# Optimization experiments

Measured on AMD Instinct MI355X. Metric: run time of the kernel, lower is better.

The kernel has to match this reference:

```python
import jax, jax.numpy as jnp
import numpy as np

NUM_BLOCKS = 2
RES_LAYERS = 10
HID = 128
IN_CH = 256
MID_CH = 512
OUT_CH = 256
DILATIONS = [2 ** l for b in range(NUM_BLOCKS) for l in range(RES_LAYERS)]
GOOD = sum(DILATIONS)  # 2046
NLAYERS = NUM_BLOCKS * RES_LAYERS


def setup_inputs() -> dict:
    key = jax.random.key(0)
    ks = jax.random.split(key, 16)
    s = 0.05
    B, T = 8, 8192
    inp = {
        "inputs": jax.random.normal(ks[0], (B, IN_CH, T), dtype=jnp.float32),
        "Wi": jax.random.normal(ks[1], (HID, IN_CH), dtype=jnp.float32) * s,
        "bi": jax.random.normal(ks[2], (HID,), dtype=jnp.float32) * s,
        "Wf": jax.random.normal(ks[3], (NLAYERS, HID, HID, 2), dtype=jnp.float32) * s,
        "bf": jax.random.normal(ks[4], (NLAYERS, HID), dtype=jnp.float32) * s,
        "Wg": jax.random.normal(ks[5], (NLAYERS, HID, HID, 2), dtype=jnp.float32) * s,
        "bg": jax.random.normal(ks[6], (NLAYERS, HID), dtype=jnp.float32) * s,
        "Wr": jax.random.normal(ks[7], (NLAYERS, HID, HID), dtype=jnp.float32) * s,
        "br": jax.random.normal(ks[8], (NLAYERS, HID), dtype=jnp.float32) * s,
        "W1": jax.random.normal(ks[9], (MID_CH, HID), dtype=jnp.float32) * s,
        "b1": jax.random.normal(ks[10], (MID_CH,), dtype=jnp.float32) * s,
        "W2": jax.random.normal(ks[11], (OUT_CH, MID_CH), dtype=jnp.float32) * s,
        "b2": jax.random.normal(ks[12], (OUT_CH,), dtype=jnp.float32) * s,
    }
    return inp


def _dilated_k2(x, W, b, d):
    # x: [B, C, T] -> [B, C, T-d]
    y = jnp.einsum("oi,bit->bot", W[:, :, 0], x[:, :, :-d]) \
        + jnp.einsum("oi,bit->bot", W[:, :, 1], x[:, :, d:])
    return y + b[None, :, None]


def reference(inputs, Wi, bi, Wf, bf, Wg, bg, Wr, br, W1, b1, W2, b2):
    T = inputs.shape[2]
    target = T - GOOD
    res = jnp.einsum("oi,bit->bot", Wi, inputs) + bi[None, :, None]
    final = None
    for idx, d in enumerate(DILATIONS):
        f = jnp.tanh(_dilated_k2(res, Wf[idx], bf[idx], d))
        g = jax.nn.sigmoid(_dilated_k2(res, Wg[idx], bg[idx], d))
        out = f * g
        x = jnp.einsum("oi,bit->bot", Wr[idx], out) + br[idx][None, :, None]
        res = x + res[:, :, d:]
        # NOTE: original code computes split conv then immediately overwrites
        # it with x[:, :, -target:]; the split conv is dead code, so skip it.
        skip = x[:, :, -target:]
        final = skip if final is None else final + skip
    h = jax.nn.relu(final)
    h = jnp.einsum("oi,bit->bot", W1, h) + b1[None, :, None]
    h = jax.nn.relu(h)
    h = jnp.einsum("oi,bit->bot", W2, h) + b2[None, :, None]
    n, c, l = h.shape
    return jnp.transpose(h, (0, 2, 1)).reshape(n * l, c)
```

## Files before the change

### kernel.cpp

```cpp
#include <hip/hip_runtime.h>


#define TT 8192
#define HIDC 128
#define GOODC 2046
#define TGT 6146
#define NL 20
#define TILE 128
#define NTB 64
#define NTILES 512
#define NBLK 512
#define GATE_CAP (1 << 18)
#define RDV_CAP (1 << 16)

typedef _Float16 half8_t __attribute__((ext_vector_type(8)));
typedef _Float16 half4_t __attribute__((ext_vector_type(4)));
typedef float floatx4 __attribute__((ext_vector_type(4)));

__device__ int g_progress[NTILES];
__device__ int g_qhead[8];
__device__ int g_arrive;
__device__ int g_broken;

__device__ __forceinline__ floatx4 mfma16(half8_t a, half8_t b, floatx4 c) {
  return __builtin_amdgcn_mfma_f32_16x16x32_f16(a, b, c, 0, 0, 0);
}
__device__ __forceinline__ float fast_sigmoid(float x) {
  return __builtin_amdgcn_rcpf(1.0f + __expf(-x));
}
__device__ __forceinline__ float fast_tanh(float x) {
  return 2.0f * __builtin_amdgcn_rcpf(1.0f + __expf(-2.0f * x)) - 1.0f;
}

__device__ __forceinline__ void cload8(
    const void* p0, const void* p1, const void* p2, const void* p3,
    const void* p4, const void* p5, const void* p6, const void* p7,
    floatx4& r0, floatx4& r1, floatx4& r2, floatx4& r3,
    floatx4& r4, floatx4& r5, floatx4& r6, floatx4& r7) {
  asm volatile(
      "global_load_dwordx4 %0, %8, off sc0\n\t"
      "global_load_dwordx4 %1, %9, off sc0\n\t"
      "global_load_dwordx4 %2, %10, off sc0\n\t"
      "global_load_dwordx4 %3, %11, off sc0\n\t"
      "global_load_dwordx4 %4, %12, off sc0\n\t"
      "global_load_dwordx4 %5, %13, off sc0\n\t"
      "global_load_dwordx4 %6, %14, off sc0\n\t"
      "global_load_dwordx4 %7, %15, off sc0\n\t"
      "s_waitcnt vmcnt(0)"
      : "=&v"(r0), "=&v"(r1), "=&v"(r2), "=&v"(r3),
        "=&v"(r4), "=&v"(r5), "=&v"(r6), "=&v"(r7)
      : "v"(p0), "v"(p1), "v"(p2), "v"(p3),
        "v"(p4), "v"(p5), "v"(p6), "v"(p7)
      : "memory");
}
__device__ __forceinline__ void cload4(const void* p0, const void* p1,
                                       const void* p2, const void* p3,
                                       floatx4& r0, floatx4& r1, floatx4& r2,
                                       floatx4& r3) {
  asm volatile(
      "global_load_dwordx4 %0, %4, off sc0\n\t"
      "global_load_dwordx4 %1, %5, off sc0\n\t"
      "global_load_dwordx4 %2, %6, off sc0\n\t"
      "global_load_dwordx4 %3, %7, off sc0\n\t"
      "s_waitcnt vmcnt(0)"
      : "=&v"(r0), "=&v"(r1), "=&v"(r2), "=&v"(r3)
      : "v"(p0), "v"(p1), "v"(p2), "v"(p3)
      : "memory");
}

__device__ __forceinline__ void spin_tile(int idx, int q) {
  int* f = &g_progress[idx];
  int it = 0;
  while (__hip_atomic_load(f, __ATOMIC_RELAXED, __HIP_MEMORY_SCOPE_AGENT) < q) {
    if (!(++it & 15) && __hip_atomic_load(&g_broken, __ATOMIC_RELAXED,
                                          __HIP_MEMORY_SCOPE_AGENT))
      break;
    if (it > GATE_CAP) {
      __hip_atomic_store(&g_broken, 1, __ATOMIC_RELAXED,
                         __HIP_MEMORY_SCOPE_AGENT);
      break;
    }
    __builtin_amdgcn_s_sleep(1);
  }
}

__global__ void prep_kernel(const float* __restrict__ Wi, const float* __restrict__ Wf,
                            const float* __restrict__ Wg, const float* __restrict__ Wr,
                            const float* __restrict__ W1, const float* __restrict__ W2,
                            _Float16* __restrict__ WIh, _Float16* __restrict__ WFG,
                            _Float16* __restrict__ WRh, _Float16* __restrict__ W1h,
                            _Float16* __restrict__ W2h) {
  int idx = blockIdx.x * blockDim.x + threadIdx.x;
  int stride = gridDim.x * blockDim.x;
  for (int i = idx; i < NTILES; i += stride) g_progress[i] = 0;
  for (int i = idx; i < 8; i += stride) g_qhead[i] = 0;
  if (idx == 0) { g_arrive = 0; g_broken = 0; }
  for (int i = idx; i < NL * 256 * 256; i += stride) {
    int l = i >> 16; int m = (i >> 8) & 255; int k = i & 255;
    int tap = k >> 7; int ci = k & 127;
    float v;
    if (m < 128) v = Wf[(((size_t)l * 128 + m) * 128 + ci) * 2 + tap];
    else         v = Wg[(((size_t)l * 128 + (m - 128)) * 128 + ci) * 2 + tap];
    WFG[i] = (_Float16)v;
  }
  for (int i = idx; i < NL * 128 * 128; i += stride) WRh[i] = (_Float16)Wr[i];
  for (int i = idx; i < 128 * 256; i += stride) WIh[i] = (_Float16)Wi[i];
  for (int i = idx; i < 512 * 128; i += stride) W1h[i] = (_Float16)W1[i];
  for (int i = idx; i < 256 * 512; i += stride) W2h[i] = (_Float16)W2[i];
}

__device__ __forceinline__ void input_half(
    const float* __restrict__ ib, const _Float16* __restrict__ WIh,
    const float* __restrict__ bi, _Float16* __restrict__ R0g,
    _Float16* __restrict__ pbout, int u0t, int h, char* smem) {
  _Float16(*Rown)[136] = (_Float16(*)[136])smem;
  _Float16(*Xs)[264] = (_Float16(*)[264])(smem + 34816);
  const int u0 = u0t + 64 * h;
  const int tid = threadIdx.x;
  const int lane = tid & 63;
  const int w = tid >> 6;
  const int ml = lane & 15;
  const int mq = lane >> 4;

#pragma unroll
  for (int it = 0; it < 4; ++it) {
    int i = it * 256 + tid;
    int n4 = i & 15;
    int kg = i >> 4;
    const float* src = ib + (size_t)(kg * 4) * TT + u0 + n4 * 4;
    floatx4 c0 = *(const floatx4*)(src);
    floatx4 c1 = *(const floatx4*)(src + TT);
    floatx4 c2 = *(const floatx4*)(src + 2 * TT);
    floatx4 c3 = *(const floatx4*)(src + 3 * TT);
#pragma unroll
    for (int tq = 0; tq < 4; ++tq) {
      half4_t hh;
      hh[0] = (_Float16)c0[tq]; hh[1] = (_Float16)c1[tq];
      hh[2] = (_Float16)c2[tq]; hh[3] = (_Float16)c3[tq];
      *(half4_t*)&Xs[n4 * 4 + tq][kg * 4] = hh;
    }
  }
  __syncthreads();

  floatx4 acc[2][4];
#pragma unroll
  for (int a = 0; a < 2; ++a)
#pragma unroll
    for (int c = 0; c < 4; ++c) acc[a][c] = floatx4{0.f, 0.f, 0.f, 0.f};
  const _Float16* Aw = WIh + (size_t)(32 * w + ml) * 256;
#pragma unroll
  for (int kk = 0; kk < 8; ++kk) {
    const int ko = kk * 32 + mq * 8;
    half8_t a0 = *(const half8_t*)(Aw + ko);
    half8_t a1 = *(const half8_t*)(Aw + 16 * 256 + ko);
#pragma unroll
    for (int nt = 0; nt < 4; ++nt) {
      half8_t bv = *(const half8_t*)&Xs[nt * 16 + ml][ko];
      acc[0][nt] = mfma16(a0, bv, acc[0][nt]);
      acc[1][nt] = mfma16(a1, bv, acc[1][nt]);
    }
  }
  __syncthreads();
  float* Xf = (float*)(smem + 34816);
#pragma unroll
  for (int mt = 0; mt < 2; ++mt) {
    const int mb = 32 * w + mt * 16 + mq * 4;
#pragma unroll
    for (int nt = 0; nt < 4; ++nt)
      *(floatx4*)&Xf[(nt * 16 + ml) * 132 + mb] = acc[mt][nt];
  }
  __syncthreads();
#pragma unroll
  for (int it = 0; it < 4; ++it) {
    int i = it * 256 + tid;
    int n = i >> 4; int cq = i & 15;
    floatx4 x0 = *(const floatx4*)&Xf[n * 132 + cq * 8];
    floatx4 x1 = *(const floatx4*)&Xf[n * 132 + cq * 8 + 4];
    floatx4 b0 = *(const floatx4*)(bi + cq * 8);
    floatx4 b1v = *(const floatx4*)(bi + cq * 8 + 4);
    half8_t hh;
#pragma unroll
    for (int tq = 0; tq < 4; ++tq) {
      hh[tq] = (_Float16)(x0[tq] + b0[tq]);
      hh[4 + tq] = (_Float16)(x1[tq] + b1v[tq]);
    }
    *(half8_t*)&Rown[64 * h + n][cq * 8] = hh;
    *(half8_t*)(R0g + (size_t)(u0 + n) * HIDC + cq * 8) = hh;
    if (h == 1 && n == 63)
      *(half8_t*)(pbout + (size_t)(u0 + n) * HIDC + cq * 8) = hh;
  }
  __syncthreads();
}

__device__ __forceinline__ void phase_layer(
    const _Float16* __restrict__ pbin, _Float16* __restrict__ pbout,
    const _Float16* __restrict__ WFGl, const _Float16* __restrict__ WRl,
    const float* __restrict__ bfl, const float* __restrict__ bgl,
    const float* __restrict__ brl, int d, int u0, int ext, char* smem) {
  _Float16(*Rown)[136] = (_Float16(*)[136])smem;
  _Float16(*Xs0)[136] = (_Float16(*)[136])(smem + 34816);
  const int tid = threadIdx.x;
  const int lane = tid & 63;
  const int w = tid >> 6;
  const int ml = lane & 15;
  const int mq = lane >> 4;

  const int dd = d < TILE ? d : TILE;
  const int nch = dd << 4;
  {
    const void* sp[8];
#pragma unroll
    for (int k = 0; k < 8; ++k) {
      int i = tid + (k << 8);
      int row = i >> 4, cc = i & 15;
      int p = u0 - d + row;
      if (p < 0) p = 0;
      sp[k] = (i < nch) ? (const void*)(pbin + (size_t)p * HIDC + cc * 8)
                        : (const void*)pbin;
    }
    floatx4 rr0, rr1, rr2, rr3, rr4, rr5, rr6, rr7;
    cload8(sp[0], sp[1], sp[2], sp[3], sp[4], sp[5], sp[6], sp[7],
           rr0, rr1, rr2, rr3, rr4, rr5, rr6, rr7);
    floatx4 rr[8] = {rr0, rr1, rr2, rr3, rr4, rr5, rr6, rr7};
#pragma unroll
    for (int k = 0; k < 8; ++k) {
      int i = tid + (k << 8);
      if (i < nch) *(floatx4*)&Xs0[i >> 4][(i & 15) * 8] = rr[k];
    }
  }
  __syncthreads();

  const _Float16* brow0[8];
  const _Float16* brow1[8];
#pragma unroll
  for (int nt = 0; nt < 8; ++nt) {
    int n = nt * 16 + ml;
    brow1[nt] = &Rown[n][0];
    brow0[nt] = (n < dd) ? &Xs0[n][0] : &Rown[n - d][0];
  }

  floatx4 accF[2][8], accG[2][8];
#pragma unroll
  for (int a = 0; a < 2; ++a)
#pragma unroll
    for (int cc = 0; cc < 8; ++cc) {
      accF[a][cc] = floatx4{0.f, 0.f, 0.f, 0.f};
      accG[a][cc] = floatx4{0.f, 0.f, 0.f, 0.f};
    }
  const _Float16* Af = WFGl + (size_t)(32 * w + ml) * 256;
  const _Float16* Ag = Af + 128 * 256;
#pragma unroll
  for (int h = 0; h < 2; ++h) {
#pragma unroll
    for (int kk = 0; kk < 4; ++kk) {
      const int ko = kk * 32 + mq * 8;
      const int kw = h * 128 + ko;
      half8_t aF0 = *(const half8_t*)(Af + kw);
      half8_t aF1 = *(const half8_t*)(Af + 16 * 256 + kw);
      half8_t aG0 = *(const half8_t*)(Ag + kw);
      half8_t aG1 = *(const half8_t*)(Ag + 16 * 256 + kw);
#pragma unroll
      for (int nt = 0; nt < 8; ++nt) {
        half8_t bv = *(const half8_t*)((h ? brow1[nt] : brow0[nt]) + ko);
        accF[0][nt] = mfma16(aF0, bv, accF[0][nt]);
        accF[1][nt] = mfma16(aF1, bv, accF[1][nt]);
        accG[0][nt] = mfma16(aG0, bv, accG[0][nt]);
        accG[1][nt] = mfma16(aG1, bv, accG[1][nt]);
      }
    }
  }

  half4_t og[2][8];
#pragma unroll
  for (int mt = 0; mt < 2; ++mt) {
    const int mb = 32 * w + mt * 16 + mq * 4;
    floatx4 bfv = *(const floatx4*)(bfl + mb);
    floatx4 bgv = *(const floatx4*)(bgl + mb);
#pragma unroll
    for (int nt = 0; nt < 8; ++nt) {
#pragma unroll
      for (int r = 0; r < 4; ++r) {
        float fv = fast_tanh(accF[mt][nt][r] + bfv[r]);
        float gv = fast_sigmoid(accG[mt][nt][r] + bgv[r]);
        og[mt][nt][r] = (_Float16)(fv * gv);
      }
    }
  }
  __syncthreads();

  _Float16(*Os)[136] = Xs0;
#pragma unroll
  for (int mt = 0; mt < 2; ++mt) {
    const int mb = 32 * w + mt * 16 + mq * 4;
#pragma unroll
    for (int nt = 0; nt < 8; ++nt)
      *(half4_t*)&Os[nt * 16 + ml][mb] = og[mt][nt];
  }
  __syncthreads();

  floatx4 accX[2][8];
#pragma unroll
  for (int a = 0; a < 2; ++a)
#pragma unroll
    for (int cc = 0; cc < 8; ++cc) accX[a][cc] = floatx4{0.f, 0.f, 0.f, 0.f};
  const _Float16* Ar = WRl + (size_t)(32 * w + ml) * 128;
#pragma unroll
  for (int kk = 0; kk < 4; ++kk) {
    const int ko = kk * 32 + mq * 8;
    half8_t a0 = *(const half8_t*)(Ar + ko);
    half8_t a1 = *(const half8_t*)(Ar + 16 * 128 + ko);
#pragma unroll
    for (int nt = 0; nt < 8; ++nt) {
      half8_t bv = *(const half8_t*)&Os[nt * 16 + ml][ko];
      accX[0][nt] = mfma16(a0, bv, accX[0][nt]);
      accX[1][nt] = mfma16(a1, bv, accX[1][nt]);
    }
  }

  half4_t xo[2][8];
#pragma unroll
  for (int mt = 0; mt < 2; ++mt) {
    const int mb = 32 * w + mt * 16 + mq * 4;
    floatx4 brv = *(const floatx4*)(brl + mb);
#pragma unroll
    for (int nt = 0; nt < 8; ++nt) {
      const int n = nt * 16 + ml;
      half4_t rold = *(const half4_t*)&Rown[n][mb];
#pragma unroll
      for (int r = 0; r < 4; ++r)
        xo[mt][nt][r] = (_Float16)(accX[mt][nt][r] + brv[r] + (float)rold[r]);
    }
  }
  __syncthreads();

#pragma unroll
  for (int mt = 0; mt < 2; ++mt) {
    const int mb = 32 * w + mt * 16 + mq * 4;
#pragma unroll
    for (int nt = 0; nt < 8; ++nt)
      *(half4_t*)&Rown[nt * 16 + ml][mb] = xo[mt][nt];
  }
  __syncthreads();

  for (int i = tid; i < (ext << 4); i += 256) {
    int row = TILE - ext + (i >> 4);
    int cc = i & 15;
    *(half8_t*)(pbout + (size_t)(u0 + row) * HIDC + cc * 8) =
        *(const half8_t*)&Rown[row][cc * 8];
  }
}

__device__ __forceinline__ void head_half(
    const _Float16* __restrict__ R0g, const _Float16* __restrict__ W1h,
    const _Float16* __restrict__ W2h, const float* __restrict__ b1,
    const float* __restrict__ b2, float* __restrict__ outb, int u0t, int h,
    char* smem) {
  _Float16(*Rown)[136] = (_Float16(*)[136])smem;
  _Float16* Hs = (_Float16*)(smem + 34816);
  _Float16* H1s = (_Float16*)(smem + 34816 + 17408);
  const int u0 = u0t + 64 * h;
  const int tid = threadIdx.x;
  const int lane = tid & 63;
  const int w = tid >> 6;
  const int ml = lane & 15;
  const int mq = lane >> 4;

  {
    const void* sp[4];
#pragma unroll
    for (int it = 0; it < 4; ++it) {
      int i = it * 256 + tid;
      sp[it] = R0g + (size_t)(u0 + (i >> 4)) * HIDC + (i & 15) * 8;
    }
    floatx4 z0, z1, z2, z3;
    cload4(sp[0], sp[1], sp[2], sp[3], z0, z1, z2, z3);
    floatx4 zz[4] = {z0, z1, z2, z3};
#pragma unroll
    for (int it = 0; it < 4; ++it) {
      int i = it * 256 + tid;
      int n = i >> 4; int cq = i & 15;
      half8_t a = *(const half8_t*)&Rown[64 * h + n][cq * 8];
      half8_t zv = *(half8_t*)&zz[it];
      half8_t hh;
#pragma unroll
      for (int tq = 0; tq < 8; ++tq) {
        float v = (float)a[tq] - (float)zv[tq];
        hh[tq] = (_Float16)(v > 0.f ? v : 0.f);
      }
      *(half8_t*)&Hs[n * 136 + cq * 8] = hh;
    }
  }
  __syncthreads();

  floatx4 accO[4][4];
#pragma unroll
  for (int a = 0; a < 4; ++a)
#pragma unroll
    for (int c = 0; c < 4; ++c) accO[a][c] = floatx4{0.f, 0.f, 0.f, 0.f};

  for (int p = 0; p < 4; ++p) {
    floatx4 acc1[2][4];
#pragma unroll
    for (int a = 0; a < 2; ++a)
#pragma unroll
      for (int c = 0; c < 4; ++c) acc1[a][c] = floatx4{0.f, 0.f, 0.f, 0.f};
    const _Float16* A1 = W1h + (size_t)(128 * p + 32 * w + ml) * 128;
#pragma unroll
    for (int kk = 0; kk < 4; ++kk) {
      const int ko = kk * 32 + mq * 8;
      half8_t av0 = *(const half8_t*)(A1 + ko);
      half8_t av1 = *(const half8_t*)(A1 + 16 * 128 + ko);
#pragma unroll
      for (int nt = 0; nt < 4; ++nt) {
        half8_t bv = *(const half8_t*)&Hs[(nt * 16 + ml) * 136 + ko];
        acc1[0][nt] = mfma16(av0, bv, acc1[0][nt]);
        acc1[1][nt] = mfma16(av1, bv, acc1[1][nt]);
      }
    }
    __syncthreads();
#pragma unroll
    for (int mt = 0; mt < 2; ++mt) {
      const int kc = 32 * w + mt * 16 + mq * 4;
      floatx4 bv = *(const floatx4*)(b1 + 128 * p + kc);
#pragma unroll
      for (int nt = 0; nt < 4; ++nt) {
        half4_t hh;
#pragma unroll
        for (int r = 0; r < 4; ++r) {
          float v = acc1[mt][nt][r] + bv[r];
          hh[r] = (_Float16)(v > 0.f ? v : 0.f);
        }
        *(half4_t*)&H1s[(nt * 16 + ml) * 136 + kc] = hh;
      }
    }
    __syncthreads();
    const _Float16* A2 = W2h + (size_t)(64 * w + ml) * 512 + p * 128;
#pragma unroll
    for (int kk = 0; kk < 4; ++kk) {
      const int ko = kk * 32 + mq * 8;
#pragma unroll
      for (int nt = 0; nt < 4; ++nt) {
        half8_t bv = *(const half8_t*)&H1s[(nt * 16 + ml) * 136 + ko];
#pragma unroll
        for (int mt = 0; mt < 4; ++mt) {
          half8_t av = *(const half8_t*)(A2 + (size_t)(mt * 16) * 512 + ko);
          accO[mt][nt] = mfma16(av, bv, accO[mt][nt]);
        }
      }
    }
    __syncthreads();
  }

  _Float16* Ot = (_Float16*)(smem + 34816);
#pragma unroll
  for (int mt = 0; mt < 4; ++mt) {
    const int m = 64 * w + mt * 16 + mq * 4;
    floatx4 bv = *(const floatx4*)(b2 + m);
#pragma unroll
    for (int nt = 0; nt < 4; ++nt) {
      const int n = nt * 16 + ml;
      half4_t hh;
#pragma unroll
      for (int r = 0; r < 4; ++r) hh[r] = (_Float16)(accO[mt][nt][r] + bv[r]);
      *(half4_t*)&Ot[n * 264 + m] = hh;
    }
  }
  __syncthreads();
#pragma unroll
  for (int it = 0; it < 8; ++it) {
    int i = it * 256 + tid;
    int n = i >> 5;
    int g = i & 31;
    int u = u0 + n;
    if (u >= GOODC) {
      half8_t v = *(const half8_t*)&Ot[n * 264 + g * 8];
      float* dst = outb + (size_t)(u - GOODC) * 256 + g * 8;
      floatx4 v0, v1;
#pragma unroll
      for (int tq = 0; tq < 4; ++tq) { v0[tq] = (float)v[tq]; v1[tq] = (float)v[4 + tq]; }
      *(floatx4*)dst = v0;
      *(floatx4*)(dst + 4) = v1;
    }
  }
  __syncthreads();
}

__global__ __launch_bounds__(256, 2) void mega_kernel(
    const float* __restrict__ inp, const _Float16* __restrict__ WIh,
    const float* __restrict__ bi, const _Float16* __restrict__ WFG,
    const _Float16* __restrict__ WRh, const float* __restrict__ bf,
    const float* __restrict__ bg, const float* __restrict__ br,
    const _Float16* __restrict__ W1h, const _Float16* __restrict__ W2h,
    const float* __restrict__ b1, const float* __restrict__ b2,
    _Float16* __restrict__ R0g, _Float16* __restrict__ Ph,
    _Float16* __restrict__ Qh, float* __restrict__ out) {
  __shared__ __align__(16) char smem[69632];
  __shared__ int s_j, s_bb, s_light;
  const int tid = threadIdx.x;

  if (tid == 0) {
    unsigned xcd;
    asm volatile("s_getreg_b32 %0, hwreg(HW_REG_XCC_ID)" : "=s"(xcd));
    xcd &= 7;
    int slot = __hip_atomic_fetch_add(&g_qhead[xcd], 1, __ATOMIC_RELAXED,
                                      __HIP_MEMORY_SCOPE_AGENT);
    __hip_atomic_fetch_add(&g_arrive, 1, __ATOMIC_RELEASE,
                           __HIP_MEMORY_SCOPE_AGENT);
    int ok = 1, it = 0;
    while (__hip_atomic_load(&g_arrive, __ATOMIC_ACQUIRE,
                             __HIP_MEMORY_SCOPE_AGENT) < NBLK) {
      if (++it > RDV_CAP) {
        ok = 0;
        __hip_atomic_store(&g_broken, 1, __ATOMIC_RELAXED,
                           __HIP_MEMORY_SCOPE_AGENT);
        break;
      }
      __builtin_amdgcn_s_sleep(8);
    }
    int light = ok;
    if (ok) {
#pragma unroll
      for (int x = 0; x < 8; ++x)
        light &= (__hip_atomic_load(&g_qhead[x], __ATOMIC_RELAXED,
                                    __HIP_MEMORY_SCOPE_AGENT) == NBLK / 8);
    }
    if (light) { s_bb = (int)xcd; s_j = slot; }
    else       { s_bb = blockIdx.x >> 6; s_j = blockIdx.x & 63; }
    s_light = light;
  }
  __syncthreads();
  const int j = s_j;
  const int bb = s_bb;
  const int light = s_light;
  const int u0 = j * TILE;

  _Float16* R0b = R0g + (size_t)bb * TT * HIDC;
  _Float16* Phb = Ph + (size_t)bb * TT * HIDC;
  _Float16* Qhb = Qh + (size_t)bb * TT * HIDC;
  const float* ib = inp + (size_t)bb * 256 * TT;
  float* outb = out + (size_t)bb * TGT * 256;
  int* myflag = &g_progress[bb * NTB + j];

#pragma unroll 1
  for (int q = 0; q < 22; ++q) {
    if (q >= 1 && q <= 20) {
      const int dcur = 1 << ((q - 1) % 10);
      const int jraw = j - ((dcur + TILE - 1) >> 7);
      int jwar = -1;
      if (q >= 2) {
        const int dp = 1 << ((q - 2) % 10);
        int cand = j + ((dp + TILE - 1) >> 7);
        if (cand <= NTB - 1) jwar = cand;
      }
      if (tid == 0 && jraw >= 0) spin_tile(bb * NTB + jraw, q);
      if (tid == 1 && jwar >= 0) spin_tile(bb * NTB + jwar, q);
      __syncthreads();
      if (!light) __builtin_amdgcn_fence(__ATOMIC_ACQUIRE, "agent");
    }

    if (q == 0) {
      input_half(ib, WIh, bi, R0b, Qhb, u0, 0, smem);
      input_half(ib, WIh, bi, R0b, Qhb, u0, 1, smem);
    } else if (q <= 20) {
      const int l = q - 1;
      const int d = 1 << (l % 10);
      const _Float16* pbin = ((q - 1) & 1) ? Phb : Qhb;
      _Float16* pbout = (q & 1) ? Phb : Qhb;
      int ext = 0;
      if (q <= 19) {
        ext = 1 << (q % 10);
        if (ext > TILE) ext = TILE;
      }
      phase_layer(pbin, pbout, WFG + (size_t)l * 65536,
                  WRh + (size_t)l * 16384, bf + l * 128, bg + l * 128,
                  br + l * 128, d, u0, ext, smem);
    } else {
      if (u0 + 127 >= GOODC) {
        if (u0 + 63 >= GOODC)
          head_half(R0b, W1h, W2h, b1, b2, outb, u0, 0, smem);
        head_half(R0b, W1h, W2h, b1, b2, outb, u0, 1, smem);
      }
    }

    if (q <= 20) {
      if (light) {
        asm volatile("s_waitcnt vmcnt(0)" ::: "memory");
      } else {
        __builtin_amdgcn_fence(__ATOMIC_RELEASE, "agent");
      }
      __syncthreads();
      if (tid == 0)
        __hip_atomic_store(myflag, q + 1, __ATOMIC_RELAXED,
                           __HIP_MEMORY_SCOPE_AGENT);
    }
  }
}

extern "C" void kernel_launch(void* const* d_in, const int* in_sizes, int n_in,
                              void* d_out, int out_size, void* d_ws, size_t ws_size,
                              hipStream_t stream) {
  const float* inputs = (const float*)d_in[0];
  const float* Wi = (const float*)d_in[1];
  const float* bi = (const float*)d_in[2];
  const float* Wf = (const float*)d_in[3];
  const float* bf = (const float*)d_in[4];
  const float* Wg = (const float*)d_in[5];
  const float* bg = (const float*)d_in[6];
  const float* Wr = (const float*)d_in[7];
  const float* br = (const float*)d_in[8];
  const float* W1 = (const float*)d_in[9];
  const float* b1 = (const float*)d_in[10];
  const float* W2 = (const float*)d_in[11];
  const float* b2 = (const float*)d_in[12];
  float* out = (float*)d_out;

  char* ws = (char*)d_ws;
  _Float16* R0g = (_Float16*)(ws + 0);
  _Float16* Ph  = (_Float16*)(ws + 16777216);
  _Float16* Qh  = (_Float16*)(ws + 33554432);
  _Float16* WFG = (_Float16*)(ws + 50331648);
  _Float16* WRh = (_Float16*)(ws + 52953088);
  _Float16* WIh = (_Float16*)(ws + 53608448);
  _Float16* W1h = (_Float16*)(ws + 53673984);
  _Float16* W2h = (_Float16*)(ws + 53805056);

  prep_kernel<<<dim3(512), dim3(256), 0, stream>>>(Wi, Wf, Wg, Wr, W1, W2,
                                                   WIh, WFG, WRh, W1h, W2h);
  mega_kernel<<<dim3(NBLK), dim3(256), 0, stream>>>(
      inputs, WIh, bi, WFG, WRh, bf, bg, br, W1h, W2h, b1, b2,
      R0g, Ph, Qh, out);
}
```

Baseline: 834.7 us.

## Triple-buffer halo slabs to relax WAR dependencies and store halos directly from registers

Adds a third ping-pong slab for the per-layer halo exchange when the workspace is large enough. A tile then waits on its downstream neighbour's progress from one layer further back, which loosens the write-after-read gate. The halo rows are written to global memory straight from registers instead of through an extra shared-memory pass and sync. It also uses the input-projection buffer directly as the layer-1 input, checks the broken flag less often while spinning, and skips the last flag store. This adds workspace-size-dependent behaviour and a more complex dependency calculation that must stay correct.

```diff
diff --git a/kernel.cpp b/kernel.cpp
--- a/kernel.cpp
+++ b/kernel.cpp
@@ -72,8 +72,8 @@
   int* f = &g_progress[idx];
   int it = 0;
   while (__hip_atomic_load(f, __ATOMIC_RELAXED, __HIP_MEMORY_SCOPE_AGENT) < q) {
-    if (!(++it & 15) && __hip_atomic_load(&g_broken, __ATOMIC_RELAXED,
-                                          __HIP_MEMORY_SCOPE_AGENT))
+    if (!(++it & 255) && __hip_atomic_load(&g_broken, __ATOMIC_RELAXED,
+                                           __HIP_MEMORY_SCOPE_AGENT))
       break;
     if (it > GATE_CAP) {
       __hip_atomic_store(&g_broken, 1, __ATOMIC_RELAXED,
@@ -112,7 +112,7 @@
 __device__ __forceinline__ void input_half(
     const float* __restrict__ ib, const _Float16* __restrict__ WIh,
     const float* __restrict__ bi, _Float16* __restrict__ R0g,
-    _Float16* __restrict__ pbout, int u0t, int h, char* smem) {
+    int u0t, int h, char* smem) {
   _Float16(*Rown)[136] = (_Float16(*)[136])smem;
   _Float16(*Xs)[264] = (_Float16(*)[264])(smem + 34816);
   const int u0 = u0t + 64 * h;
@@ -186,8 +186,6 @@
     }
     *(half8_t*)&Rown[64 * h + n][cq * 8] = hh;
     *(half8_t*)(R0g + (size_t)(u0 + n) * HIDC + cq * 8) = hh;
-    if (h == 1 && n == 63)
-      *(half8_t*)(pbout + (size_t)(u0 + n) * HIDC + cq * 8) = hh;
   }
   __syncthreads();
 }
@@ -331,6 +329,18 @@
         xo[mt][nt][r] = (_Float16)(accX[mt][nt][r] + brv[r] + (float)rold[r]);
     }
   }
+  if (ext > 0) {
+#pragma unroll
+    for (int mt = 0; mt < 2; ++mt) {
+      const int mb = 32 * w + mt * 16 + mq * 4;
+#pragma unroll
+      for (int nt = 0; nt < 8; ++nt) {
+        const int n = nt * 16 + ml;
+        if (n >= TILE - ext)
+          *(half4_t*)(pbout + (size_t)(u0 + n) * HIDC + mb) = xo[mt][nt];
+      }
+    }
+  }
   __syncthreads();
 
 #pragma unroll
@@ -339,14 +349,6 @@
 #pragma unroll
     for (int nt = 0; nt < 8; ++nt)
       *(half4_t*)&Rown[nt * 16 + ml][mb] = xo[mt][nt];
-  }
-  __syncthreads();
-
-  for (int i = tid; i < (ext << 4); i += 256) {
-    int row = TILE - ext + (i >> 4);
-    int cc = i & 15;
-    *(half8_t*)(pbout + (size_t)(u0 + row) * HIDC + cc * 8) =
-        *(const half8_t*)&Rown[row][cc * 8];
   }
 }
 
@@ -492,8 +494,9 @@
     const float* __restrict__ bg, const float* __restrict__ br,
     const _Float16* __restrict__ W1h, const _Float16* __restrict__ W2h,
     const float* __restrict__ b1, const float* __restrict__ b2,
-    _Float16* __restrict__ R0g, _Float16* __restrict__ Ph,
-    _Float16* __restrict__ Qh, float* __restrict__ out) {
+    _Float16* __restrict__ R0g, _Float16* __restrict__ Ah,
+    _Float16* __restrict__ Bh, _Float16* __restrict__ Ch,
+    float* __restrict__ out, int nslots) {
   __shared__ __align__(16) char smem[69632];
   __shared__ int s_j, s_bb, s_light;
   const int tid = threadIdx.x;
@@ -535,8 +538,8 @@
   const int u0 = j * TILE;
 
   _Float16* R0b = R0g + (size_t)bb * TT * HIDC;
-  _Float16* Phb = Ph + (size_t)bb * TT * HIDC;
-  _Float16* Qhb = Qh + (size_t)bb * TT * HIDC;
+  _Float16* sl[3] = {Ah + (size_t)bb * TT * HIDC, Bh + (size_t)bb * TT * HIDC,
+                     Ch + (size_t)bb * TT * HIDC};
   const float* ib = inp + (size_t)bb * 256 * TT;
   float* outb = out + (size_t)bb * TGT * 256;
   int* myflag = &g_progress[bb * NTB + j];
@@ -544,28 +547,29 @@
 #pragma unroll 1
   for (int q = 0; q < 22; ++q) {
     if (q >= 1 && q <= 20) {
-      const int dcur = 1 << ((q - 1) % 10);
-      const int jraw = j - ((dcur + TILE - 1) >> 7);
-      int jwar = -1;
-      if (q >= 2) {
-        const int dp = 1 << ((q - 2) % 10);
+      const int dq = 1 << ((q - 1) % 10);
+      const int jraw = j - ((dq + TILE - 1) >> 7);
+      int jwar = -1, warq = 0;
+      if (q > nslots) {
+        const int p = q - nslots + 1;
+        const int dp = 1 << ((p - 1) % 10);
         int cand = j + ((dp + TILE - 1) >> 7);
-        if (cand <= NTB - 1) jwar = cand;
+        if (cand <= NTB - 1) { jwar = cand; warq = q - nslots + 2; }
       }
       if (tid == 0 && jraw >= 0) spin_tile(bb * NTB + jraw, q);
-      if (tid == 1 && jwar >= 0) spin_tile(bb * NTB + jwar, q);
+      if (tid == 1 && jwar >= 0) spin_tile(bb * NTB + jwar, warq);
       __syncthreads();
       if (!light) __builtin_amdgcn_fence(__ATOMIC_ACQUIRE, "agent");
     }
 
     if (q == 0) {
-      input_half(ib, WIh, bi, R0b, Qhb, u0, 0, smem);
-      input_half(ib, WIh, bi, R0b, Qhb, u0, 1, smem);
+      input_half(ib, WIh, bi, R0b, u0, 0, smem);
+      input_half(ib, WIh, bi, R0b, u0, 1, smem);
     } else if (q <= 20) {
       const int l = q - 1;
       const int d = 1 << (l % 10);
-      const _Float16* pbin = ((q - 1) & 1) ? Phb : Qhb;
-      _Float16* pbout = (q & 1) ? Phb : Qhb;
+      const _Float16* pbin = (q == 1) ? R0b : sl[(q - 2) % nslots];
+      _Float16* pbout = sl[(q - 1) % nslots];
       int ext = 0;
       if (q <= 19) {
         ext = 1 << (q % 10);
@@ -589,7 +593,7 @@
         __builtin_amdgcn_fence(__ATOMIC_RELEASE, "agent");
       }
       __syncthreads();
-      if (tid == 0)
+      if (q <= 19 && tid == 0)
         __hip_atomic_store(myflag, q + 1, __ATOMIC_RELAXED,
                            __HIP_MEMORY_SCOPE_AGENT);
     }
@@ -614,19 +618,23 @@
   const float* b2 = (const float*)d_in[12];
   float* out = (float*)d_out;
 
+  const size_t SLAB = 16777216;
+  int nslots = (ws_size >= 4 * SLAB + 4194304) ? 3 : 2;
   char* ws = (char*)d_ws;
   _Float16* R0g = (_Float16*)(ws + 0);
-  _Float16* Ph  = (_Float16*)(ws + 16777216);
-  _Float16* Qh  = (_Float16*)(ws + 33554432);
-  _Float16* WFG = (_Float16*)(ws + 50331648);
-  _Float16* WRh = (_Float16*)(ws + 52953088);
-  _Float16* WIh = (_Float16*)(ws + 53608448);
-  _Float16* W1h = (_Float16*)(ws + 53673984);
-  _Float16* W2h = (_Float16*)(ws + 53805056);
+  _Float16* Ah  = (_Float16*)(ws + SLAB);
+  _Float16* Bh  = (_Float16*)(ws + 2 * SLAB);
+  _Float16* Ch  = (_Float16*)(ws + (nslots == 3 ? 3 * SLAB : 2 * SLAB));
+  char* wb = ws + (size_t)(nslots == 3 ? 4 : 3) * SLAB;
+  _Float16* WFG = (_Float16*)(wb);
+  _Float16* WRh = (_Float16*)(wb + 2621440);
+  _Float16* WIh = (_Float16*)(wb + 3276800);
+  _Float16* W1h = (_Float16*)(wb + 3342336);
+  _Float16* W2h = (_Float16*)(wb + 3473408);
 
   prep_kernel<<<dim3(512), dim3(256), 0, stream>>>(Wi, Wf, Wg, Wr, W1, W2,
                                                    WIh, WFG, WRh, W1h, W2h);
   mega_kernel<<<dim3(NBLK), dim3(256), 0, stream>>>(
       inputs, WIh, bi, WFG, WRh, bf, bg, br, W1h, W2h, b1, b2,
-      R0g, Ph, Qh, out);
-}
+      R0g, Ah, Bh, Ch, out, nslots);
+}
```

Measured after the change: 895.4 us. 1.07x slower.

## Halve time tile to 64 and run 1024 persistent blocks with padded flags

Applied to the files above, without the earlier changes.

Shrinks each block's time tile from 128 to 64 columns and doubles the grid to 1024 blocks at 4 blocks per CU, cutting shared memory per block in half. The layer halo is now written straight from registers, the input stage no longer seeds the ping-pong buffer, and layer 1 reads R0 directly. Progress flags are padded to separate cache lines, and the broken-flag check in the spin loop runs less often. The aim is more parallelism and less false sharing on flags, at the cost of more dependency waits and more halo loads per unit of work.

```diff
diff --git a/kernel.cpp b/kernel.cpp
--- a/kernel.cpp
+++ b/kernel.cpp
@@ -6,10 +6,11 @@
 #define GOODC 2046
 #define TGT 6146
 #define NL 20
-#define TILE 128
-#define NTB 64
-#define NTILES 512
-#define NBLK 512
+#define TILE 64
+#define NTB 128
+#define NTILES 1024
+#define NBLK 1024
+#define FPAD 32
 #define GATE_CAP (1 << 18)
 #define RDV_CAP (1 << 16)
 
@@ -17,7 +18,7 @@
 typedef _Float16 half4_t __attribute__((ext_vector_type(4)));
 typedef float floatx4 __attribute__((ext_vector_type(4)));
 
-__device__ int g_progress[NTILES];
+__device__ int g_progress[NTILES * FPAD];
 __device__ int g_qhead[8];
 __device__ int g_arrive;
 __device__ int g_broken;
@@ -32,27 +33,6 @@
   return 2.0f * __builtin_amdgcn_rcpf(1.0f + __expf(-2.0f * x)) - 1.0f;
 }
 
-__device__ __forceinline__ void cload8(
-    const void* p0, const void* p1, const void* p2, const void* p3,
-    const void* p4, const void* p5, const void* p6, const void* p7,
-    floatx4& r0, floatx4& r1, floatx4& r2, floatx4& r3,
-    floatx4& r4, floatx4& r5, floatx4& r6, floatx4& r7) {
-  asm volatile(
-      "global_load_dwordx4 %0, %8, off sc0\n\t"
-      "global_load_dwordx4 %1, %9, off sc0\n\t"
-      "global_load_dwordx4 %2, %10, off sc0\n\t"
-      "global_load_dwordx4 %3, %11, off sc0\n\t"
-      "global_load_dwordx4 %4, %12, off sc0\n\t"
-      "global_load_dwordx4 %5, %13, off sc0\n\t"
-      "global_load_dwordx4 %6, %14, off sc0\n\t"
-      "global_load_dwordx4 %7, %15, off sc0\n\t"
-      "s_waitcnt vmcnt(0)"
-      : "=&v"(r0), "=&v"(r1), "=&v"(r2), "=&v"(r3),
-        "=&v"(r4), "=&v"(r5), "=&v"(r6), "=&v"(r7)
-      : "v"(p0), "v"(p1), "v"(p2), "v"(p3),
-        "v"(p4), "v"(p5), "v"(p6), "v"(p7)
-      : "memory");
-}
 __device__ __forceinline__ void cload4(const void* p0, const void* p1,
                                        const void* p2, const void* p3,
                                        floatx4& r0, floatx4& r1, floatx4& r2,
@@ -69,11 +49,11 @@
 }
 
 __device__ __forceinline__ void spin_tile(int idx, int q) {
-  int* f = &g_progress[idx];
+  int* f = &g_progress[idx * FPAD];
   int it = 0;
   while (__hip_atomic_load(f, __ATOMIC_RELAXED, __HIP_MEMORY_SCOPE_AGENT) < q) {
-    if (!(++it & 15) && __hip_atomic_load(&g_broken, __ATOMIC_RELAXED,
-                                          __HIP_MEMORY_SCOPE_AGENT))
+    if (!(++it & 255) && __hip_atomic_load(&g_broken, __ATOMIC_RELAXED,
+                                           __HIP_MEMORY_SCOPE_AGENT))
       break;
     if (it > GATE_CAP) {
       __hip_atomic_store(&g_broken, 1, __ATOMIC_RELAXED,
@@ -92,7 +72,7 @@
                             _Float16* __restrict__ W2h) {
   int idx = blockIdx.x * blockDim.x + threadIdx.x;
   int stride = gridDim.x * blockDim.x;
-  for (int i = idx; i < NTILES; i += stride) g_progress[i] = 0;
+  for (int i = idx; i < NTILES * FPAD; i += stride) g_progress[i] = 0;
   for (int i = idx; i < 8; i += stride) g_qhead[i] = 0;
   if (idx == 0) { g_arrive = 0; g_broken = 0; }
   for (int i = idx; i < NL * 256 * 256; i += stride) {
@@ -109,13 +89,13 @@
   for (int i = idx; i < 256 * 512; i += stride) W2h[i] = (_Float16)W2[i];
 }
 
-__device__ __forceinline__ void input_half(
+__device__ __forceinline__ void input_chunk(
     const float* __restrict__ ib, const _Float16* __restrict__ WIh,
     const float* __restrict__ bi, _Float16* __restrict__ R0g,
-    _Float16* __restrict__ pbout, int u0t, int h, char* smem) {
+    int u0t, int ch, char* smem) {
   _Float16(*Rown)[136] = (_Float16(*)[136])smem;
-  _Float16(*Xs)[264] = (_Float16(*)[264])(smem + 34816);
-  const int u0 = u0t + 64 * h;
+  _Float16(*Xs)[264] = (_Float16(*)[264])(smem + 17408);
+  const int u0 = u0t + 32 * ch;
   const int tid = threadIdx.x;
   const int lane = tid & 63;
   const int w = tid >> 6;
@@ -123,10 +103,10 @@
   const int mq = lane >> 4;
 
 #pragma unroll
-  for (int it = 0; it < 4; ++it) {
+  for (int it = 0; it < 2; ++it) {
     int i = it * 256 + tid;
-    int n4 = i & 15;
-    int kg = i >> 4;
+    int n4 = i & 7;
+    int kg = i >> 3;
     const float* src = ib + (size_t)(kg * 4) * TT + u0 + n4 * 4;
     floatx4 c0 = *(const floatx4*)(src);
     floatx4 c1 = *(const floatx4*)(src + TT);
@@ -142,11 +122,11 @@
   }
   __syncthreads();
 
-  floatx4 acc[2][4];
+  floatx4 acc[2][2];
 #pragma unroll
   for (int a = 0; a < 2; ++a)
 #pragma unroll
-    for (int c = 0; c < 4; ++c) acc[a][c] = floatx4{0.f, 0.f, 0.f, 0.f};
+    for (int c = 0; c < 2; ++c) acc[a][c] = floatx4{0.f, 0.f, 0.f, 0.f};
   const _Float16* Aw = WIh + (size_t)(32 * w + ml) * 256;
 #pragma unroll
   for (int kk = 0; kk < 8; ++kk) {
@@ -154,24 +134,24 @@
     half8_t a0 = *(const half8_t*)(Aw + ko);
     half8_t a1 = *(const half8_t*)(Aw + 16 * 256 + ko);
 #pragma unroll
-    for (int nt = 0; nt < 4; ++nt) {
+    for (int nt = 0; nt < 2; ++nt) {
       half8_t bv = *(const half8_t*)&Xs[nt * 16 + ml][ko];
       acc[0][nt] = mfma16(a0, bv, acc[0][nt]);
       acc[1][nt] = mfma16(a1, bv, acc[1][nt]);
     }
   }
   __syncthreads();
-  float* Xf = (float*)(smem + 34816);
+  float* Xf = (float*)(smem + 17408);
 #pragma unroll
   for (int mt = 0; mt < 2; ++mt) {
     const int mb = 32 * w + mt * 16 + mq * 4;
 #pragma unroll
-    for (int nt = 0; nt < 4; ++nt)
+    for (int nt = 0; nt < 2; ++nt)
       *(floatx4*)&Xf[(nt * 16 + ml) * 132 + mb] = acc[mt][nt];
   }
   __syncthreads();
 #pragma unroll
-  for (int it = 0; it < 4; ++it) {
+  for (int it = 0; it < 2; ++it) {
     int i = it * 256 + tid;
     int n = i >> 4; int cq = i & 15;
     floatx4 x0 = *(const floatx4*)&Xf[n * 132 + cq * 8];
@@ -184,10 +164,8 @@
       hh[tq] = (_Float16)(x0[tq] + b0[tq]);
       hh[4 + tq] = (_Float16)(x1[tq] + b1v[tq]);
     }
-    *(half8_t*)&Rown[64 * h + n][cq * 8] = hh;
+    *(half8_t*)&Rown[32 * ch + n][cq * 8] = hh;
     *(half8_t*)(R0g + (size_t)(u0 + n) * HIDC + cq * 8) = hh;
-    if (h == 1 && n == 63)
-      *(half8_t*)(pbout + (size_t)(u0 + n) * HIDC + cq * 8) = hh;
   }
   __syncthreads();
 }
@@ -198,7 +176,7 @@
     const float* __restrict__ bfl, const float* __restrict__ bgl,
     const float* __restrict__ brl, int d, int u0, int ext, char* smem) {
   _Float16(*Rown)[136] = (_Float16(*)[136])smem;
-  _Float16(*Xs0)[136] = (_Float16(*)[136])(smem + 34816);
+  _Float16(*Xs0)[136] = (_Float16(*)[136])(smem + 17408);
   const int tid = threadIdx.x;
   const int lane = tid & 63;
   const int w = tid >> 6;
@@ -208,9 +186,9 @@
   const int dd = d < TILE ? d : TILE;
   const int nch = dd << 4;
   {
-    const void* sp[8];
-#pragma unroll
-    for (int k = 0; k < 8; ++k) {
+    const void* sp[4];
+#pragma unroll
+    for (int k = 0; k < 4; ++k) {
       int i = tid + (k << 8);
       int row = i >> 4, cc = i & 15;
       int p = u0 - d + row;
@@ -218,32 +196,31 @@
       sp[k] = (i < nch) ? (const void*)(pbin + (size_t)p * HIDC + cc * 8)
                         : (const void*)pbin;
     }
-    floatx4 rr0, rr1, rr2, rr3, rr4, rr5, rr6, rr7;
-    cload8(sp[0], sp[1], sp[2], sp[3], sp[4], sp[5], sp[6], sp[7],
-           rr0, rr1, rr2, rr3, rr4, rr5, rr6, rr7);
-    floatx4 rr[8] = {rr0, rr1, rr2, rr3, rr4, rr5, rr6, rr7};
-#pragma unroll
-    for (int k = 0; k < 8; ++k) {
+    floatx4 r0, r1, r2, r3;
+    cload4(sp[0], sp[1], sp[2], sp[3], r0, r1, r2, r3);
+    floatx4 rr[4] = {r0, r1, r2, r3};
+#pragma unroll
+    for (int k = 0; k < 4; ++k) {
       int i = tid + (k << 8);
       if (i < nch) *(floatx4*)&Xs0[i >> 4][(i & 15) * 8] = rr[k];
     }
   }
   __syncthreads();
 
-  const _Float16* brow0[8];
-  const _Float16* brow1[8];
-#pragma unroll
-  for (int nt = 0; nt < 8; ++nt) {
+  const _Float16* brow0[4];
+  const _Float16* brow1[4];
+#pragma unroll
+  for (int nt = 0; nt < 4; ++nt) {
     int n = nt * 16 + ml;
     brow1[nt] = &Rown[n][0];
     brow0[nt] = (n < dd) ? &Xs0[n][0] : &Rown[n - d][0];
   }
 
-  floatx4 accF[2][8], accG[2][8];
+  floatx4 accF[2][4], accG[2][4];
 #pragma unroll
   for (int a = 0; a < 2; ++a)
 #pragma unroll
-    for (int cc = 0; cc < 8; ++cc) {
+    for (int cc = 0; cc < 4; ++cc) {
       accF[a][cc] = floatx4{0.f, 0.f, 0.f, 0.f};
       accG[a][cc] = floatx4{0.f, 0.f, 0.f, 0.f};
     }
@@ -260,7 +237,7 @@
       half8_t aG0 = *(const half8_t*)(Ag + kw);
       half8_t aG1 = *(const half8_t*)(Ag + 16 * 256 + kw);
 #pragma unroll
-      for (int nt = 0; nt < 8; ++nt) {
+      for (int nt = 0; nt < 4; ++nt) {
         half8_t bv = *(const half8_t*)((h ? brow1[nt] : brow0[nt]) + ko);
         accF[0][nt] = mfma16(aF0, bv, accF[0][nt]);
         accF[1][nt] = mfma16(aF1, bv, accF[1][nt]);
@@ -270,14 +247,14 @@
     }
   }
 
-  half4_t og[2][8];
+  half4_t og[2][4];
 #pragma unroll
   for (int mt = 0; mt < 2; ++mt) {
     const int mb = 32 * w + mt * 16 + mq * 4;
     floatx4 bfv = *(const floatx4*)(bfl + mb);
     floatx4 bgv = *(const floatx4*)(bgl + mb);
 #pragma unroll
-    for (int nt = 0; nt < 8; ++nt) {
+    for (int nt = 0; nt < 4; ++nt) {
 #pragma unroll
       for (int r = 0; r < 4; ++r) {
         float fv = fast_tanh(accF[mt][nt][r] + bfv[r]);
@@ -293,16 +270,16 @@
   for (int mt = 0; mt < 2; ++mt) {
     const int mb = 32 * w + mt * 16 + mq * 4;
 #pragma unroll
-    for (int nt = 0; nt < 8; ++nt)
+    for (int nt = 0; nt < 4; ++nt)
       *(half4_t*)&Os[nt * 16 + ml][mb] = og[mt][nt];
   }
   __syncthreads();
 
-  floatx4 accX[2][8];
+  floatx4 accX[2][4];
 #pragma unroll
   for (int a = 0; a < 2; ++a)
 #pragma unroll
-    for (int cc = 0; cc < 8; ++cc) accX[a][cc] = floatx4{0.f, 0.f, 0.f, 0.f};
+    for (int cc = 0; cc < 4; ++cc) accX[a][cc] = floatx4{0.f, 0.f, 0.f, 0.f};
   const _Float16* Ar = WRl + (size_t)(32 * w + ml) * 128;
 #pragma unroll
   for (int kk = 0; kk < 4; ++kk) {
@@ -310,20 +287,20 @@
     half8_t a0 = *(const half8_t*)(Ar + ko);
     half8_t a1 = *(const half8_t*)(Ar + 16 * 128 + ko);
 #pragma unroll
-    for (int nt = 0; nt < 8; ++nt) {
+    for (int nt = 0; nt < 4; ++nt) {
       half8_t bv = *(const half8_t*)&Os[nt * 16 + ml][ko];
       accX[0][nt] = mfma16(a0, bv, accX[0][nt]);
       accX[1][nt] = mfma16(a1, bv, accX[1][nt]);
     }
   }
 
-  half4_t xo[2][8];
+  half4_t xo[2][4];
 #pragma unroll
   for (int mt = 0; mt < 2; ++mt) {
     const int mb = 32 * w + mt * 16 + mq * 4;
     floatx4 brv = *(const floatx4*)(brl + mb);
 #pragma unroll
-    for (int nt = 0; nt < 8; ++nt) {
+    for (int nt = 0; nt < 4; ++nt) {
       const int n = nt * 16 + ml;
       half4_t rold = *(const half4_t*)&Rown[n][mb];
 #pragma unroll
@@ -331,34 +308,36 @@
         xo[mt][nt][r] = (_Float16)(accX[mt][nt][r] + brv[r] + (float)rold[r]);
     }
   }
+  if (ext > 0) {
+#pragma unroll
+    for (int mt = 0; mt < 2; ++mt) {
+      const int mb = 32 * w + mt * 16 + mq * 4;
+#pragma unroll
+      for (int nt = 0; nt < 4; ++nt) {
+        const int n = nt * 16 + ml;
+        if (n >= TILE - ext)
+          *(half4_t*)(pbout + (size_t)(u0 + n) * HIDC + mb) = xo[mt][nt];
+      }
+    }
+  }
   __syncthreads();
 
 #pragma unroll
   for (int mt = 0; mt < 2; ++mt) {
     const int mb = 32 * w + mt * 16 + mq * 4;
 #pragma unroll
-    for (int nt = 0; nt < 8; ++nt)
+    for (int nt = 0; nt < 4; ++nt)
       *(half4_t*)&Rown[nt * 16 + ml][mb] = xo[mt][nt];
   }
-  __syncthreads();
-
-  for (int i = tid; i < (ext << 4); i += 256) {
-    int row = TILE - ext + (i >> 4);
-    int cc = i & 15;
-    *(half8_t*)(pbout + (size_t)(u0 + row) * HIDC + cc * 8) =
-        *(const half8_t*)&Rown[row][cc * 8];
-  }
-}
-
-__device__ __forceinline__ void head_half(
+}
+
+__device__ __forceinline__ void head_tile(
     const _Float16* __restrict__ R0g, const _Float16* __restrict__ W1h,
     const _Float16* __restrict__ W2h, const float* __restrict__ b1,
-    const float* __restrict__ b2, float* __restrict__ outb, int u0t, int h,
+    const float* __restrict__ b2, float* __restrict__ outb, int u0,
     char* smem) {
-  _Float16(*Rown)[136] = (_Float16(*)[136])smem;
-  _Float16* Hs = (_Float16*)(smem + 34816);
-  _Float16* H1s = (_Float16*)(smem + 34816 + 17408);
-  const int u0 = u0t + 64 * h;
+  _Float16* Hs = (_Float16*)smem;
+  _Float16* H1s = (_Float16*)(smem + 17408);
   const int tid = threadIdx.x;
   const int lane = tid & 63;
   const int w = tid >> 6;
@@ -379,7 +358,7 @@
     for (int it = 0; it < 4; ++it) {
       int i = it * 256 + tid;
       int n = i >> 4; int cq = i & 15;
-      half8_t a = *(const half8_t*)&Rown[64 * h + n][cq * 8];
+      half8_t a = *(const half8_t*)&Hs[n * 136 + cq * 8];
       half8_t zv = *(half8_t*)&zz[it];
       half8_t hh;
 #pragma unroll
@@ -451,7 +430,7 @@
     __syncthreads();
   }
 
-  _Float16* Ot = (_Float16*)(smem + 34816);
+  _Float16* Ot = (_Float16*)smem;
 #pragma unroll
   for (int mt = 0; mt < 4; ++mt) {
     const int m = 64 * w + mt * 16 + mq * 4;
@@ -482,19 +461,18 @@
       *(floatx4*)(dst + 4) = v1;
     }
   }
-  __syncthreads();
-}
-
-__global__ __launch_bounds__(256, 2) void mega_kernel(
+}
+
+__global__ __launch_bounds__(256, 4) void mega_kernel(
     const float* __restrict__ inp, const _Float16* __restrict__ WIh,
     const float* __restrict__ bi, const _Float16* __restrict__ WFG,
     const _Float16* __restrict__ WRh, const float* __restrict__ bf,
     const float* __restrict__ bg, const float* __restrict__ br,
     const _Float16* __restrict__ W1h, const _Float16* __restrict__ W2h,
     const float* __restrict__ b1, const float* __restrict__ b2,
-    _Float16* __restrict__ R0g, _Float16* __restrict__ Ph,
-    _Float16* __restrict__ Qh, float* __restrict__ out) {
-  __shared__ __align__(16) char smem[69632];
+    _Float16* __restrict__ R0g, _Float16* __restrict__ Ah,
+    _Float16* __restrict__ Bh, float* __restrict__ out) {
+  __shared__ __align__(16) char smem[34816];
   __shared__ int s_j, s_bb, s_light;
   const int tid = threadIdx.x;
 
@@ -525,7 +503,7 @@
                                     __HIP_MEMORY_SCOPE_AGENT) == NBLK / 8);
     }
     if (light) { s_bb = (int)xcd; s_j = slot; }
-    else       { s_bb = blockIdx.x >> 6; s_j = blockIdx.x & 63; }
+    else       { s_bb = blockIdx.x >> 7; s_j = blockIdx.x & 127; }
     s_light = light;
   }
   __syncthreads();
@@ -535,21 +513,20 @@
   const int u0 = j * TILE;
 
   _Float16* R0b = R0g + (size_t)bb * TT * HIDC;
-  _Float16* Phb = Ph + (size_t)bb * TT * HIDC;
-  _Float16* Qhb = Qh + (size_t)bb * TT * HIDC;
+  _Float16* sl[2] = {Ah + (size_t)bb * TT * HIDC, Bh + (size_t)bb * TT * HIDC};
   const float* ib = inp + (size_t)bb * 256 * TT;
   float* outb = out + (size_t)bb * TGT * 256;
-  int* myflag = &g_progress[bb * NTB + j];
+  int* myflag = &g_progress[(bb * NTB + j) * FPAD];
 
 #pragma unroll 1
   for (int q = 0; q < 22; ++q) {
     if (q >= 1 && q <= 20) {
-      const int dcur = 1 << ((q - 1) % 10);
-      const int jraw = j - ((dcur + TILE - 1) >> 7);
+      const int dq = 1 << ((q - 1) % 10);
+      const int jraw = j - ((dq + TILE - 1) >> 6);
       int jwar = -1;
-      if (q >= 2) {
+      if (q >= 3) {
         const int dp = 1 << ((q - 2) % 10);
-        int cand = j + ((dp + TILE - 1) >> 7);
+        int cand = j + ((dp + TILE - 1) >> 6);
         if (cand <= NTB - 1) jwar = cand;
       }
       if (tid == 0 && jraw >= 0) spin_tile(bb * NTB + jraw, q);
@@ -559,13 +536,13 @@
     }
 
     if (q == 0) {
-      input_half(ib, WIh, bi, R0b, Qhb, u0, 0, smem);
-      input_half(ib, WIh, bi, R0b, Qhb, u0, 1, smem);
+      input_chunk(ib, WIh, bi, R0b, u0, 0, smem);
+      input_chunk(ib, WIh, bi, R0b, u0, 1, smem);
     } else if (q <= 20) {
       const int l = q - 1;
       const int d = 1 << (l % 10);
-      const _Float16* pbin = ((q - 1) & 1) ? Phb : Qhb;
-      _Float16* pbout = (q & 1) ? Phb : Qhb;
+      const _Float16* pbin = (q == 1) ? R0b : sl[(q - 2) & 1];
+      _Float16* pbout = sl[(q - 1) & 1];
       int ext = 0;
       if (q <= 19) {
         ext = 1 << (q % 10);
@@ -575,11 +552,8 @@
                   WRh + (size_t)l * 16384, bf + l * 128, bg + l * 128,
                   br + l * 128, d, u0, ext, smem);
     } else {
-      if (u0 + 127 >= GOODC) {
-        if (u0 + 63 >= GOODC)
-          head_half(R0b, W1h, W2h, b1, b2, outb, u0, 0, smem);
-        head_half(R0b, W1h, W2h, b1, b2, outb, u0, 1, smem);
-      }
+      if (u0 + TILE - 1 >= GOODC)
+        head_tile(R0b, W1h, W2h, b1, b2, outb, u0, smem);
     }
 
     if (q <= 20) {
@@ -589,7 +563,7 @@
         __builtin_amdgcn_fence(__ATOMIC_RELEASE, "agent");
       }
       __syncthreads();
-      if (tid == 0)
+      if (q <= 19 && tid == 0)
         __hip_atomic_store(myflag, q + 1, __ATOMIC_RELAXED,
                            __HIP_MEMORY_SCOPE_AGENT);
     }
@@ -616,8 +590,8 @@
 
   char* ws = (char*)d_ws;
   _Float16* R0g = (_Float16*)(ws + 0);
-  _Float16* Ph  = (_Float16*)(ws + 16777216);
-  _Float16* Qh  = (_Float16*)(ws + 33554432);
+  _Float16* Ah  = (_Float16*)(ws + 16777216);
+  _Float16* Bh  = (_Float16*)(ws + 33554432);
   _Float16* WFG = (_Float16*)(ws + 50331648);
   _Float16* WRh = (_Float16*)(ws + 52953088);
   _Float16* WIh = (_Float16*)(ws + 53608448);
@@ -628,5 +602,5 @@
                                                    WIh, WFG, WRh, W1h, W2h);
   mega_kernel<<<dim3(NBLK), dim3(256), 0, stream>>>(
       inputs, WIh, bi, WFG, WRh, bf, bg, br, W1h, W2h, b1, b2,
-      R0g, Ph, Qh, out);
-}
+      R0g, Ah, Bh, out);
+}
```

Result: slower. 1.000 ms (+19.8%).
